# Kernel tuning notes

Hardware: AMD Instinct MI355X
Metric: run time of the kernel (lower is better)

## Reference

```python
import jax, jax.numpy as jnp
import numpy as np

BN_EPS = 1e-5

def setup_inputs() -> dict:
    key = jax.random.key(0)
    ks = jax.random.split(key, 12)
    B, C, H, W = 8, 512, 56, 56
    IC = 256  # inter_channels = in_channels // 2
    s_in = 1.0 / np.sqrt(C)
    s_ic = 1.0 / np.sqrt(IC)
    return {
        "x": jax.random.normal(ks[0], (B, C, H, W), dtype=jnp.float32),
        "theta_w": jax.random.normal(ks[1], (IC, C), dtype=jnp.float32) * s_in,
        "theta_b": jax.random.normal(ks[2], (IC,), dtype=jnp.float32) * s_in,
        "phi_w": jax.random.normal(ks[3], (IC, C), dtype=jnp.float32) * s_in,
        "phi_b": jax.random.normal(ks[4], (IC,), dtype=jnp.float32) * s_in,
        "g_w": jax.random.normal(ks[5], (IC, C), dtype=jnp.float32) * s_in,
        "g_b": jax.random.normal(ks[6], (IC,), dtype=jnp.float32) * s_in,
        "wz_w": jax.random.normal(ks[7], (C, IC), dtype=jnp.float32) * s_ic,
        "wz_b": jax.random.normal(ks[8], (C,), dtype=jnp.float32) * s_ic,
        "bn_w": jax.random.normal(ks[9], (C,), dtype=jnp.float32) * 0.1,
        "bn_b": jax.random.normal(ks[10], (C,), dtype=jnp.float32) * 0.1,
    }


def reference(x, theta_w, theta_b, phi_w, phi_b, g_w, g_b, wz_w, wz_b, bn_w, bn_b):
    B, C, H, W = x.shape
    N = H * W
    # [B, N, C] tokens
    xf = x.reshape(B, C, N).transpose(0, 2, 1)
    Q = jnp.einsum('bnc,ic->bni', xf, theta_w) + theta_b   # [B, N, IC]
    K = jnp.einsum('bnc,ic->bni', xf, phi_w) + phi_b       # [B, N, IC]
    V = jnp.einsum('bnc,ic->bni', xf, g_w) + g_b           # [B, N, IC]
    attn = jax.nn.softmax(jnp.einsum('bqi,bki->bqk', Q, K), axis=-1)  # [B, N, N]
    y = jnp.einsum('bqk,bki->bqi', attn, V)                # [B, N, IC]
    y = jnp.einsum('bqi,ci->bqc', y, wz_w) + wz_b          # [B, N, C]
    y = y.transpose(0, 2, 1).reshape(B, C, H, W)
    # BatchNorm2d, training-mode batch stats (biased variance)
    mean = jnp.mean(y, axis=(0, 2, 3))
    var = jnp.var(y, axis=(0, 2, 3))
    yn = (y - mean[None, :, None, None]) * jax.lax.rsqrt(var + BN_EPS)[None, :, None, None]
    y = yn * bn_w[None, :, None, None] + bn_b[None, :, None, None]
    return y + x
```

## Files before the change

kernel.cpp:

```cpp
#include <hip/hip_runtime.h>
#include <math.h>

#define B_  8
#define C_  512
#define N_  3136
#define IC_ 256
#define NPART 784

typedef __attribute__((ext_vector_type(8))) short bf16x8;
typedef __attribute__((ext_vector_type(4))) float f32x4;
typedef __attribute__((ext_vector_type(16))) float f32x16;

static __device__ __forceinline__ unsigned short f2bf(float f) {
    unsigned int u = __builtin_bit_cast(unsigned int, f);
    u = (u + 0x7fffu + ((u >> 16) & 1u)) >> 16;
    return (unsigned short)u;
}
static __device__ __forceinline__ float bf2f(unsigned short u) {
    return __builtin_bit_cast(float, (unsigned int)u << 16);
}
static __device__ __forceinline__ unsigned int pk2(float a, float b) {
    return (unsigned int)f2bf(a) | ((unsigned int)f2bf(b) << 16);
}

static __device__ __forceinline__ void gll16(const unsigned short* g, unsigned short* l) {
    __builtin_amdgcn_global_load_lds(
        (const __attribute__((address_space(1))) unsigned int*)g,
        (__attribute__((address_space(3))) unsigned int*)l, 16, 0, 0);
}

__global__ __launch_bounds__(256) void xpose_kernel(
    const float* __restrict__ x, unsigned short* __restrict__ xb)
{
    const int n0 = blockIdx.x * 64;
    const int c0 = blockIdx.y * 64;
    const int b  = blockIdx.z;
    __shared__ unsigned short T[64][72];
    const int tid = threadIdx.x;
#pragma unroll
    for (int e = 0; e < 4; ++e) {
        const int idx = tid + e * 256;
        const int row = idx >> 4;
        const int c4  = idx & 15;
        const float4 v = *(const float4*)&x[((size_t)b * C_ + c0 + row) * N_ + n0 + c4 * 4];
        T[c4 * 4 + 0][row] = f2bf(v.x);
        T[c4 * 4 + 1][row] = f2bf(v.y);
        T[c4 * 4 + 2][row] = f2bf(v.z);
        T[c4 * 4 + 3][row] = f2bf(v.w);
    }
    __syncthreads();
#pragma unroll
    for (int e = 0; e < 2; ++e) {
        const int s  = tid + e * 256;
        const int nr = s >> 3;
        const int sl = s & 7;
        *(bf16x8*)&xb[((size_t)b * N_ + n0 + nr) * C_ + c0 + sl * 8] =
            *(const bf16x8*)&T[nr][sl * 8];
    }
}

__global__ __launch_bounds__(256) void wconv_kernel(
    const float* __restrict__ tw, const float* __restrict__ pw,
    const float* __restrict__ gw, const float* __restrict__ wzw,
    unsigned short* __restrict__ Wcat, unsigned short* __restrict__ wzwb)
{
    const int gid = blockIdx.x * 256 + threadIdx.x;
    if (gid < 98304) {
        const int i  = gid >> 7;
        const int c4 = gid & 127;
        const float* src = (i < 256) ? &tw[(size_t)i * 512]
                         : (i < 512) ? &pw[(size_t)(i - 256) * 512]
                                     : &gw[(size_t)(i - 512) * 512];
        const float4 v = *(const float4*)&src[c4 * 4];
        ushort4 o; o.x = f2bf(v.x); o.y = f2bf(v.y); o.z = f2bf(v.z); o.w = f2bf(v.w);
        *(ushort4*)&Wcat[(size_t)i * 512 + c4 * 4] = o;
    } else {
        const int g2 = gid - 98304;
        const int r  = g2 >> 6;
        const int c4 = g2 & 63;
        const float4 v = *(const float4*)&wzw[(size_t)r * 256 + c4 * 4];
        ushort4 o; o.x = f2bf(v.x); o.y = f2bf(v.y); o.z = f2bf(v.z); o.w = f2bf(v.w);
        *(ushort4*)&wzwb[(size_t)r * 256 + c4 * 4] = o;
    }
}

__global__ __launch_bounds__(256, 2) void qkv_mfma_kernel(
    const unsigned short* __restrict__ xb, const unsigned short* __restrict__ Wcat,
    const float* __restrict__ tb, const float* __restrict__ pb,
    const float* __restrict__ gb,
    unsigned short* __restrict__ Q, unsigned short* __restrict__ K,
    unsigned short* __restrict__ Vt)
{
    const int n0 = blockIdx.x * 64;
    const int by = blockIdx.y;
    const int b  = blockIdx.z;
    const int i0 = by * 128;
    const int tid = threadIdx.x;
    const int wq = tid >> 6, lane = tid & 63;
    const int g = lane >> 4, c = lane & 15;
    const int wm = wq >> 1, wn = wq & 1;

    __shared__ unsigned short smem[12288];
    unsigned short* Asm = smem;
    unsigned short* Bsm = smem + 4096;

    const int srow = tid >> 3;
    const int ssl  = tid & 7;

    f32x4 acc[2][4];
#pragma unroll
    for (int mb = 0; mb < 2; ++mb)
#pragma unroll
        for (int nb = 0; nb < 4; ++nb) acc[mb][nb] = (f32x4){0.f, 0.f, 0.f, 0.f};

    bf16x8 ast[2], bst[4];
#pragma unroll
    for (int e = 0; e < 2; ++e) {
        const int row = srow + e * 32;
        ast[e] = *(const bf16x8*)&xb[((size_t)b * N_ + n0 + row) * C_ + ((ssl ^ (row & 7)) << 3)];
    }
#pragma unroll
    for (int e = 0; e < 4; ++e) {
        const int row = srow + e * 32;
        bst[e] = *(const bf16x8*)&Wcat[(size_t)(i0 + row) * C_ + ((ssl ^ (row & 7)) << 3)];
    }
#pragma unroll
    for (int e = 0; e < 2; ++e) *(bf16x8*)&Asm[(srow + e * 32) * 64 + ssl * 8] = ast[e];
#pragma unroll
    for (int e = 0; e < 4; ++e) *(bf16x8*)&Bsm[(srow + e * 32) * 64 + ssl * 8] = bst[e];
    __syncthreads();

    const int arow[2] = { wm * 32 + c, wm * 32 + 16 + c };
    const int brow[4] = { wn * 64 + c, wn * 64 + 16 + c, wn * 64 + 32 + c, wn * 64 + 48 + c };

    for (int s = 0; s < 8; ++s) {
        const int c0n = (s < 7) ? (s + 1) * 64 : s * 64;
#pragma unroll
        for (int e = 0; e < 2; ++e) {
            const int row = srow + e * 32;
            ast[e] = *(const bf16x8*)&xb[((size_t)b * N_ + n0 + row) * C_ + c0n + ((ssl ^ (row & 7)) << 3)];
        }
#pragma unroll
        for (int e = 0; e < 4; ++e) {
            const int row = srow + e * 32;
            bst[e] = *(const bf16x8*)&Wcat[(size_t)(i0 + row) * C_ + c0n + ((ssl ^ (row & 7)) << 3)];
        }
#pragma unroll
        for (int ks = 0; ks < 2; ++ks) {
            bf16x8 af[2], bfr[4];
            const int sl = ((ks << 2) | g);
#pragma unroll
            for (int mb = 0; mb < 2; ++mb)
                af[mb] = *(const bf16x8*)&Asm[arow[mb] * 64 + ((sl ^ (c & 7)) << 3)];
#pragma unroll
            for (int nb = 0; nb < 4; ++nb)
                bfr[nb] = *(const bf16x8*)&Bsm[brow[nb] * 64 + ((sl ^ (c & 7)) << 3)];
#pragma unroll
            for (int mb = 0; mb < 2; ++mb)
#pragma unroll
                for (int nb = 0; nb < 4; ++nb)
                    acc[mb][nb] = __builtin_amdgcn_mfma_f32_16x16x32_bf16(af[mb], bfr[nb], acc[mb][nb], 0, 0, 0);
        }
        __syncthreads();
#pragma unroll
        for (int e = 0; e < 2; ++e) *(bf16x8*)&Asm[(srow + e * 32) * 64 + ssl * 8] = ast[e];
#pragma unroll
        for (int e = 0; e < 4; ++e) *(bf16x8*)&Bsm[(srow + e * 32) * 64 + ssl * 8] = bst[e];
        __syncthreads();
    }

    const int proj = by >> 1;
    const float* bias = (proj == 0) ? tb : (proj == 1) ? pb : gb;
    const int icb = (by & 1) * 128;
    if (proj < 2) {
        unsigned short* out = (proj == 0) ? Q : K;
#pragma unroll
        for (int mb = 0; mb < 2; ++mb)
#pragma unroll
            for (int nb = 0; nb < 4; ++nb)
#pragma unroll
                for (int r = 0; r < 4; ++r) {
                    const int token = n0 + wm * 32 + mb * 16 + g * 4 + r;
                    const int ic = icb + wn * 64 + nb * 16 + c;
                    out[((size_t)b * N_ + token) * IC_ + ic] = f2bf(acc[mb][nb][r] + bias[ic]);
                }
    } else {
        unsigned short* T = smem;
#pragma unroll
        for (int mb = 0; mb < 2; ++mb)
#pragma unroll
            for (int nb = 0; nb < 4; ++nb)
#pragma unroll
                for (int r = 0; r < 4; ++r) {
                    const int il = wn * 64 + nb * 16 + c;
                    const int tl = wm * 32 + mb * 16 + g * 4 + r;
                    T[il * 72 + tl] = f2bf(acc[mb][nb][r] + bias[icb + il]);
                }
        __syncthreads();
#pragma unroll
        for (int e = 0; e < 4; ++e) {
            const int row = (tid >> 3) + e * 32;
            *(bf16x8*)&Vt[((size_t)b * IC_ + icb + row) * N_ + n0 + ((tid & 7) * 8)] =
                *(const bf16x8*)&T[row * 72 + (tid & 7) * 8];
        }
    }
}

__global__ __launch_bounds__(512, 2) void attn_kernel(
    const unsigned short* __restrict__ Q, const unsigned short* __restrict__ K,
    const unsigned short* __restrict__ Vt,
    unsigned short* __restrict__ part, float2* __restrict__ ml)
{
    const int b     = blockIdx.x;
    const int qb    = blockIdx.y;
    const int split = blockIdx.z;
    int q0 = qb * 256; if (q0 > N_ - 256) q0 = N_ - 256;
    const int t0 = split ? 25 : 0;
    const int t1 = split ? 49 : 25;

    const int tid  = threadIdx.x;
    const int wq   = tid >> 6;
    const int lane = tid & 63;
    const int ql   = lane & 31;
    const int h    = lane >> 5;
    const int swz0 = (ql & 7) ^ (ql >> 3);

    const unsigned short* Qb = Q  + (size_t)b * N_ * IC_;
    const unsigned short* Kb = K  + (size_t)b * N_ * IC_;
    const unsigned short* Vb = Vt + (size_t)b * IC_ * N_;

    __shared__ unsigned short Ks[2][64 * 256];
    __shared__ unsigned short Vs[2][256 * 64];

    const int krow = tid >> 5, ksl = tid & 31;
    const int vrow = tid >> 3, vsl = tid & 7;
    const unsigned short* vg =
        Vb + (size_t)vrow * N_ + ((vsl ^ ((vrow & 7) ^ ((vrow >> 3) & 7))) << 3);

#define STAGE(buf, t)                                                            \
    {                                                                            \
        _Pragma("unroll") for (int e = 0; e < 4; ++e) {                          \
            const int kr = krow + e * 16;                                        \
            gll16(Kb + ((size_t)(t) * 64 + kr) * IC_ +                           \
                      ((ksl ^ ((kr & 7) ^ ((kr >> 3) & 7))) << 3),               \
                  &Ks[buf][(tid + e * 512) * 8]);                                \
        }                                                                        \
        const unsigned short* vgp = vg + (size_t)(t) * 64;                       \
        _Pragma("unroll") for (int e = 0; e < 4; ++e)                            \
            gll16(vgp + (size_t)e * 64 * N_, &Vs[buf][(tid + e * 512) * 8]);     \
    }

    bf16x8 qf[16];
    {
        const unsigned short* qrow = &Qb[(size_t)(q0 + wq * 32 + ql) * IC_ + h * 8];
#pragma unroll
        for (int s = 0; s < 16; ++s) qf[s] = *(const bf16x8*)&qrow[s * 16];
    }

    f32x16 yacc[8];
#pragma unroll
    for (int db = 0; db < 8; ++db)
#pragma unroll
        for (int i = 0; i < 16; ++i) yacc[db][i] = 0.f;
    float m = -1e30f, lsum = 0.f;

    STAGE(0, t0);
    asm volatile("s_waitcnt vmcnt(0)" ::: "memory");
    __syncthreads();

    for (int t = t0; t < t1; ++t) {
        const int cur = (t - t0) & 1;
        if (t + 1 < t1) STAGE(cur ^ 1, t + 1);

        f32x16 s0, s1;
#pragma unroll
        for (int i = 0; i < 16; ++i) { s0[i] = 0.f; s1[i] = 0.f; }
        __builtin_amdgcn_s_setprio(1);
#pragma unroll
        for (int s = 0; s < 16; ++s) {
            const int sl = ((2 * s + h) ^ swz0) << 3;
            const bf16x8 kf0 = *(const bf16x8*)&Ks[cur][(size_t)ql * 256 + sl];
            s0 = __builtin_amdgcn_mfma_f32_32x32x16_bf16(kf0, qf[s], s0, 0, 0, 0);
            const bf16x8 kf1 = *(const bf16x8*)&Ks[cur][(size_t)(32 + ql) * 256 + (sl ^ 32)];
            s1 = __builtin_amdgcn_mfma_f32_32x32x16_bf16(kf1, qf[s], s1, 0, 0, 0);
        }
        __builtin_amdgcn_s_setprio(0);

        float mx[16];
#pragma unroll
        for (int i = 0; i < 16; ++i) mx[i] = fmaxf(s0[i], s1[i]);
#pragma unroll
        for (int off = 8; off > 0; off >>= 1)
#pragma unroll
            for (int i = 0; i < 8; ++i)
                if (i < off) mx[i] = fmaxf(mx[i], mx[i + off]);
        float rm = fmaxf(mx[0], __shfl_xor(mx[0], 32));

        if (__any(rm > m + 8.f)) {
            const float mnew  = fmaxf(m, rm);
            const float scale = __expf(m - mnew);
            m = mnew;
            lsum *= scale;
#pragma unroll
            for (int db = 0; db < 8; ++db)
#pragma unroll
                for (int i = 0; i < 16; ++i) yacc[db][i] *= scale;
        }

#pragma unroll
        for (int i = 0; i < 16; ++i) s0[i] = __expf(s0[i] - m);
#pragma unroll
        for (int i = 0; i < 16; ++i) s1[i] = __expf(s1[i] - m);
        float sm[16];
#pragma unroll
        for (int i = 0; i < 16; ++i) sm[i] = s0[i] + s1[i];
#pragma unroll
        for (int off = 8; off > 0; off >>= 1)
#pragma unroll
            for (int i = 0; i < 8; ++i)
                if (i < off) sm[i] += sm[i + off];
        lsum += sm[0] + __shfl_xor(sm[0], 32);

        unsigned int pk0[8], pk1[8];
#pragma unroll
        for (int w = 0; w < 8; ++w) {
            pk0[w] = pk2(s0[2 * w], s0[2 * w + 1]);
            pk1[w] = pk2(s1[2 * w], s1[2 * w + 1]);
        }

#pragma unroll
        for (int s = 0; s < 4; ++s) {
            const unsigned int* u4 = (s >> 1) ? &pk1[4 * (s & 1)] : &pk0[4 * (s & 1)];
            const unsigned int send0 = h ? u4[0] : u4[2];
            const unsigned int send1 = h ? u4[1] : u4[3];
            const unsigned int r0 = (unsigned int)__shfl_xor((int)send0, 32);
            const unsigned int r1 = (unsigned int)__shfl_xor((int)send1, 32);
            uint4 fw;
            fw.x = h ? r0 : u4[0];
            fw.y = h ? r1 : u4[1];
            fw.z = h ? u4[2] : r0;
            fw.w = h ? u4[3] : r1;
            const bf16x8 pf = __builtin_bit_cast(bf16x8, fw);
            const int vsl_r = ((2 * s + h) ^ swz0) << 3;
            __builtin_amdgcn_s_setprio(1);
#pragma unroll
            for (int db = 0; db < 8; ++db) {
                const bf16x8 vf = *(const bf16x8*)
                    &Vs[cur][(size_t)(db * 32 + ql) * 64 + (vsl_r ^ (((db & 1) << 2) << 3))];
                yacc[db] = __builtin_amdgcn_mfma_f32_32x32x16_bf16(vf, pf, yacc[db], 0, 0, 0);
            }
            __builtin_amdgcn_s_setprio(0);
        }

        asm volatile("s_waitcnt vmcnt(0)" ::: "memory");
        __syncthreads();
    }

    const size_t pbase = (size_t)(b * 2 + split) * N_;
    const int q = q0 + wq * 32 + ql;
    if (h == 0) ml[pbase + q] = make_float2(m, lsum);
#pragma unroll
    for (int db = 0; db < 8; ++db)
#pragma unroll
        for (int rq = 0; rq < 4; ++rq) {
            ushort4 o;
            o.x = f2bf(yacc[db][4 * rq + 0]);
            o.y = f2bf(yacc[db][4 * rq + 1]);
            o.z = f2bf(yacc[db][4 * rq + 2]);
            o.w = f2bf(yacc[db][4 * rq + 3]);
            *(ushort4*)&part[(pbase + q) * IC_ + 32 * db + 8 * rq + 4 * h] = o;
        }
#undef STAGE
}

__global__ __launch_bounds__(256) void attn_merge_kernel(
    const unsigned short* __restrict__ part, const float2* __restrict__ ml,
    unsigned short* __restrict__ Y)
{
    const int b  = blockIdx.y;
    const int q  = blockIdx.x * 64 + (threadIdx.x >> 2);
    const int d0 = (threadIdx.x & 3) * 64;
    const float2 A  = ml[(size_t)(b * 2 + 0) * N_ + q];
    const float2 Bv = ml[(size_t)(b * 2 + 1) * N_ + q];
    const float mm = fmaxf(A.x, Bv.x);
    const float wA = __expf(A.x - mm), wB = __expf(Bv.x - mm);
    const float inv = 1.f / (A.y * wA + Bv.y * wB);
    const unsigned short* pA = &part[((size_t)(b * 2 + 0) * N_ + q) * IC_ + d0];
    const unsigned short* pB = &part[((size_t)(b * 2 + 1) * N_ + q) * IC_ + d0];
    unsigned short* y = &Y[((size_t)b * N_ + q) * IC_ + d0];
#pragma unroll
    for (int j = 0; j < 8; ++j) {
        const bf16x8 va = *(const bf16x8*)&pA[j * 8];
        const bf16x8 vb = *(const bf16x8*)&pB[j * 8];
        unsigned short o[8];
#pragma unroll
        for (int k = 0; k < 8; ++k)
            o[k] = f2bf((bf2f((unsigned short)va[k]) * wA +
                         bf2f((unsigned short)vb[k]) * wB) * inv);
        *(bf16x8*)&y[j * 8] = *(const bf16x8*)o;
    }
}

__global__ __launch_bounds__(256, 2) void wz_mfma_kernel(
    const unsigned short* __restrict__ Yb, const unsigned short* __restrict__ wzwb,
    const float* __restrict__ wzb, float* __restrict__ Z,
    float2* __restrict__ partial)
{
    const int n0 = blockIdx.x * 64;
    const int c0 = blockIdx.y * 128;
    const int b  = blockIdx.z;
    const int tid = threadIdx.x;
    const int wq = tid >> 6, lane = tid & 63;
    const int g = lane >> 4, c = lane & 15;
    const int wm = wq >> 1, wn = wq & 1;

    __shared__ unsigned short smem[12288];
    unsigned short* Asm = smem;
    unsigned short* Bsm = smem + 8192;

    const int srow = tid >> 3;
    const int ssl  = tid & 7;

    f32x4 acc[4][2];
#pragma unroll
    for (int mb = 0; mb < 4; ++mb)
#pragma unroll
        for (int nb = 0; nb < 2; ++nb) acc[mb][nb] = (f32x4){0.f, 0.f, 0.f, 0.f};

    bf16x8 ast[4], bst[2];
#pragma unroll
    for (int e = 0; e < 4; ++e) {
        const int row = srow + e * 32;
        ast[e] = *(const bf16x8*)&wzwb[(size_t)(c0 + row) * IC_ + ((ssl ^ (row & 7)) << 3)];
    }
#pragma unroll
    for (int e = 0; e < 2; ++e) {
        const int row = srow + e * 32;
        bst[e] = *(const bf16x8*)&Yb[((size_t)b * N_ + n0 + row) * IC_ + ((ssl ^ (row & 7)) << 3)];
    }
#pragma unroll
    for (int e = 0; e < 4; ++e) *(bf16x8*)&Asm[(srow + e * 32) * 64 + ssl * 8] = ast[e];
#pragma unroll
    for (int e = 0; e < 2; ++e) *(bf16x8*)&Bsm[(srow + e * 32) * 64 + ssl * 8] = bst[e];
    __syncthreads();

    const int arow[4] = { wm * 64 + c, wm * 64 + 16 + c, wm * 64 + 32 + c, wm * 64 + 48 + c };
    const int brow[2] = { wn * 32 + c, wn * 32 + 16 + c };

    for (int s = 0; s < 4; ++s) {
        const int k0n = (s < 3) ? (s + 1) * 64 : s * 64;
#pragma unroll
        for (int e = 0; e < 4; ++e) {
            const int row = srow + e * 32;
            ast[e] = *(const bf16x8*)&wzwb[(size_t)(c0 + row) * IC_ + k0n + ((ssl ^ (row & 7)) << 3)];
        }
#pragma unroll
        for (int e = 0; e < 2; ++e) {
            const int row = srow + e * 32;
            bst[e] = *(const bf16x8*)&Yb[((size_t)b * N_ + n0 + row) * IC_ + k0n + ((ssl ^ (row & 7)) << 3)];
        }
#pragma unroll
        for (int ks = 0; ks < 2; ++ks) {
            bf16x8 af[4], bfr[2];
            const int sl = ((ks << 2) | g);
#pragma unroll
            for (int mb = 0; mb < 4; ++mb)
                af[mb] = *(const bf16x8*)&Asm[arow[mb] * 64 + ((sl ^ (c & 7)) << 3)];
#pragma unroll
            for (int nb = 0; nb < 2; ++nb)
                bfr[nb] = *(const bf16x8*)&Bsm[brow[nb] * 64 + ((sl ^ (c & 7)) << 3)];
#pragma unroll
            for (int mb = 0; mb < 4; ++mb)
#pragma unroll
                for (int nb = 0; nb < 2; ++nb)
                    acc[mb][nb] = __builtin_amdgcn_mfma_f32_16x16x32_bf16(af[mb], bfr[nb], acc[mb][nb], 0, 0, 0);
        }
        __syncthreads();
#pragma unroll
        for (int e = 0; e < 4; ++e) *(bf16x8*)&Asm[(srow + e * 32) * 64 + ssl * 8] = ast[e];
#pragma unroll
        for (int e = 0; e < 2; ++e) *(bf16x8*)&Bsm[(srow + e * 32) * 64 + ssl * 8] = bst[e];
        __syncthreads();
    }

    const int slot = (b * 49 + blockIdx.x) * 2 + wn;
#pragma unroll
    for (int mb = 0; mb < 4; ++mb) {
#pragma unroll
        for (int r = 0; r < 4; ++r) {
            const int cg = c0 + wm * 64 + mb * 16 + g * 4 + r;
            const float bw = wzb[cg];
            const float z0 = acc[mb][0][r] + bw;
            const float z1 = acc[mb][1][r] + bw;
            Z[((size_t)b * C_ + cg) * N_ + n0 + wn * 32 + c]      = z0;
            Z[((size_t)b * C_ + cg) * N_ + n0 + wn * 32 + 16 + c] = z1;
            float ps = z0 + z1;
            float pq = z0 * z0 + z1 * z1;
#pragma unroll
            for (int off = 1; off <= 8; off <<= 1) {
                ps += __shfl_xor(ps, off);
                pq += __shfl_xor(pq, off);
            }
            if (c == 0) partial[(size_t)cg * NPART + slot] = make_float2(ps, pq);
        }
    }
}

__global__ __launch_bounds__(256) void bn_finalize_kernel(
    const float2* __restrict__ partial, float* __restrict__ stats)
{
    const int c   = blockIdx.x;
    const int tid = threadIdx.x;
    double s = 0.0, q = 0.0;
    for (int i = tid; i < NPART; i += 256) {
        const float2 p = partial[(size_t)c * NPART + i];
        s += p.x; q += p.y;
    }
    __shared__ double ls[256], lq[256];
    ls[tid] = s; lq[tid] = q;
    __syncthreads();
    for (int off = 128; off > 0; off >>= 1) {
        if (tid < off) { ls[tid] += ls[tid + off]; lq[tid] += lq[tid + off]; }
        __syncthreads();
    }
    if (tid == 0) {
        const double M    = (double)B_ * (double)N_;
        const double mean = ls[0] / M;
        const double var  = lq[0] / M - mean * mean;
        stats[c]      = (float)mean;
        stats[C_ + c] = (float)var;
    }
}

__global__ __launch_bounds__(256) void bn_apply_kernel(
    const float* __restrict__ Z, const float* __restrict__ x,
    const float* __restrict__ stats,
    const float* __restrict__ bnw, const float* __restrict__ bnb,
    float* __restrict__ out)
{
    const size_t total4 = (size_t)B_ * C_ * N_ / 4;
    const size_t i4 = (size_t)blockIdx.x * blockDim.x + threadIdx.x;
    if (i4 >= total4) return;
    const size_t i = i4 * 4;
    const int c = (int)((i / N_) % C_);
    const float mean = stats[c];
    const float var  = stats[C_ + c];
    const float sc = rsqrtf(var + 1e-5f) * bnw[c];
    const float sh = bnb[c] - mean * sc;
    const float4 z  = ((const float4*)Z)[i4];
    const float4 xv = ((const float4*)x)[i4];
    float4 o;
    o.x = z.x * sc + sh + xv.x;
    o.y = z.y * sc + sh + xv.y;
    o.z = z.z * sc + sh + xv.z;
    o.w = z.w * sc + sh + xv.w;
    ((float4*)out)[i4] = o;
}

extern "C" void kernel_launch(void* const* d_in, const int* in_sizes, int n_in,
                              void* d_out, int out_size, void* d_ws, size_t ws_size,
                              hipStream_t stream)
{
    const float* x   = (const float*)d_in[0];
    const float* tw  = (const float*)d_in[1];
    const float* tb  = (const float*)d_in[2];
    const float* pw  = (const float*)d_in[3];
    const float* pb  = (const float*)d_in[4];
    const float* gw  = (const float*)d_in[5];
    const float* gb  = (const float*)d_in[6];
    const float* wzw = (const float*)d_in[7];
    const float* wzb = (const float*)d_in[8];
    const float* bnw = (const float*)d_in[9];
    const float* bnb = (const float*)d_in[10];
    float* out = (float*)d_out;

    const size_t NIC = (size_t)B_ * N_ * IC_;
    const size_t BNC = (size_t)B_ * N_ * C_;
    unsigned short* Qw   = (unsigned short*)d_ws;
    unsigned short* Kw   = Qw + NIC;
    unsigned short* Vtw  = Kw + NIC;
    unsigned short* Ybw  = Vtw + NIC;
    unsigned short* xbw  = Ybw + NIC;
    unsigned short* partw = xbw;
    unsigned short* Wcat = xbw + BNC;
    unsigned short* wzwb = Wcat + 768 * 512;
    float* stats = (float*)(wzwb + 512 * 256);
    float2* mlw  = (float2*)(stats + 2 * C_);
    float2* bnpart = mlw + (size_t)B_ * 2 * N_;
    float* Zb    = out;

    wconv_kernel<<<512, 256, 0, stream>>>(tw, pw, gw, wzw, Wcat, wzwb);
    xpose_kernel<<<dim3(N_ / 64, C_ / 64, B_), 256, 0, stream>>>(x, xbw);
    qkv_mfma_kernel<<<dim3(N_ / 64, 6, B_), 256, 0, stream>>>(
        xbw, Wcat, tb, pb, gb, Qw, Kw, Vtw);
    attn_kernel<<<dim3(B_, 13, 2), 512, 0, stream>>>(Qw, Kw, Vtw, partw, mlw);
    attn_merge_kernel<<<dim3(N_ / 64, B_), 256, 0, stream>>>(partw, mlw, Ybw);
    wz_mfma_kernel<<<dim3(N_ / 64, C_ / 128, B_), 256, 0, stream>>>(Ybw, wzwb, wzb, Zb, bnpart);
    bn_finalize_kernel<<<C_, 256, 0, stream>>>(bnpart, stats);
    const int total4 = B_ * C_ * N_ / 4;
    bn_apply_kernel<<<(total4 + 255) / 256, 256, 0, stream>>>(Zb, x, stats, bnw, bnb, out);
}
```

Before: 273.2 us.

## Split attention into four KV splits with smaller query blocks, single-buffered LDS

The attention kernel moves from 512-thread blocks over 256 queries with a 2-way KV split to 256-thread blocks over 128 queries with a 4-way KV split (13/12/12/12 tiles). The grid grows from 208 to 800 blocks, which fills more CUs. Shared memory drops from double-buffered to a single buffer, so each tile's load is no longer overlapped with compute and the loop now syncs twice per tile. The merge kernel combines four partials, one of them written in place into the output buffer, which adds extra partial-buffer traffic and workspace.

After: 438.2 us. 60.4% more time.

```diff
diff --git a/kernel.cpp b/kernel.cpp
--- a/kernel.cpp
+++ b/kernel.cpp
@@ -206,17 +206,19 @@
     }
 }
 
-__global__ __launch_bounds__(512, 2) void attn_kernel(
+__global__ __launch_bounds__(256, 2) void attn_kernel(
     const unsigned short* __restrict__ Q, const unsigned short* __restrict__ K,
     const unsigned short* __restrict__ Vt,
-    unsigned short* __restrict__ part, float2* __restrict__ ml)
+    unsigned short* __restrict__ p0, unsigned short* __restrict__ p1,
+    unsigned short* __restrict__ p2, unsigned short* __restrict__ p3,
+    float2* __restrict__ ml)
 {
     const int b     = blockIdx.x;
     const int qb    = blockIdx.y;
     const int split = blockIdx.z;
-    int q0 = qb * 256; if (q0 > N_ - 256) q0 = N_ - 256;
-    const int t0 = split ? 25 : 0;
-    const int t1 = split ? 49 : 25;
+    int q0 = qb * 128; if (q0 > N_ - 128) q0 = N_ - 128;
+    const int t0 = split * 12 + (split ? 1 : 0);
+    const int t1 = t0 + (split ? 12 : 13);
 
     const int tid  = threadIdx.x;
     const int wq   = tid >> 6;
@@ -229,25 +231,26 @@
     const unsigned short* Kb = K  + (size_t)b * N_ * IC_;
     const unsigned short* Vb = Vt + (size_t)b * IC_ * N_;
 
-    __shared__ unsigned short Ks[2][64 * 256];
-    __shared__ unsigned short Vs[2][256 * 64];
-
-    const int krow = tid >> 5, ksl = tid & 31;
-    const int vrow = tid >> 3, vsl = tid & 7;
-    const unsigned short* vg =
-        Vb + (size_t)vrow * N_ + ((vsl ^ ((vrow & 7) ^ ((vrow >> 3) & 7))) << 3);
-
-#define STAGE(buf, t)                                                            \
-    {                                                                            \
-        _Pragma("unroll") for (int e = 0; e < 4; ++e) {                          \
-            const int kr = krow + e * 16;                                        \
-            gll16(Kb + ((size_t)(t) * 64 + kr) * IC_ +                           \
-                      ((ksl ^ ((kr & 7) ^ ((kr >> 3) & 7))) << 3),               \
-                  &Ks[buf][(tid + e * 512) * 8]);                                \
-        }                                                                        \
-        const unsigned short* vgp = vg + (size_t)(t) * 64;                       \
-        _Pragma("unroll") for (int e = 0; e < 4; ++e)                            \
-            gll16(vgp + (size_t)e * 64 * N_, &Vs[buf][(tid + e * 512) * 8]);     \
+    __shared__ unsigned short Ks[64 * 256];
+    __shared__ unsigned short Vs[256 * 64];
+
+    const int ksl = tid & 31;
+    const int vsl = tid & 7;
+
+#define STAGE(t)                                                               \
+    {                                                                          \
+        _Pragma("unroll") for (int e = 0; e < 8; ++e) {                        \
+            const int kr = (tid >> 5) + e * 8;                                 \
+            gll16(Kb + ((size_t)(t) * 64 + kr) * IC_ +                         \
+                      ((ksl ^ ((kr & 7) ^ ((kr >> 3) & 7))) << 3),             \
+                  &Ks[(tid + e * 256) * 8]);                                   \
+        }                                                                      \
+        _Pragma("unroll") for (int e = 0; e < 8; ++e) {                        \
+            const int vr = (tid >> 3) + e * 32;                                \
+            gll16(Vb + (size_t)vr * N_ + (size_t)(t) * 64 +                    \
+                      ((vsl ^ ((vr & 7) ^ ((vr >> 3) & 7))) << 3),             \
+                  &Vs[(tid + e * 256) * 8]);                                   \
+        }                                                                      \
     }
 
     bf16x8 qf[16];
@@ -264,13 +267,11 @@
         for (int i = 0; i < 16; ++i) yacc[db][i] = 0.f;
     float m = -1e30f, lsum = 0.f;
 
-    STAGE(0, t0);
-    asm volatile("s_waitcnt vmcnt(0)" ::: "memory");
-    __syncthreads();
-
     for (int t = t0; t < t1; ++t) {
-        const int cur = (t - t0) & 1;
-        if (t + 1 < t1) STAGE(cur ^ 1, t + 1);
+        __syncthreads();
+        STAGE(t);
+        asm volatile("s_waitcnt vmcnt(0)" ::: "memory");
+        __syncthreads();
 
         f32x16 s0, s1;
 #pragma unroll
@@ -279,9 +280,9 @@
 #pragma unroll
         for (int s = 0; s < 16; ++s) {
             const int sl = ((2 * s + h) ^ swz0) << 3;
-            const bf16x8 kf0 = *(const bf16x8*)&Ks[cur][(size_t)ql * 256 + sl];
+            const bf16x8 kf0 = *(const bf16x8*)&Ks[(size_t)ql * 256 + sl];
             s0 = __builtin_amdgcn_mfma_f32_32x32x16_bf16(kf0, qf[s], s0, 0, 0, 0);
-            const bf16x8 kf1 = *(const bf16x8*)&Ks[cur][(size_t)(32 + ql) * 256 + (sl ^ 32)];
+            const bf16x8 kf1 = *(const bf16x8*)&Ks[(size_t)(32 + ql) * 256 + (sl ^ 32)];
             s1 = __builtin_amdgcn_mfma_f32_32x32x16_bf16(kf1, qf[s], s1, 0, 0, 0);
         }
         __builtin_amdgcn_s_setprio(0);
@@ -346,19 +347,16 @@
 #pragma unroll
             for (int db = 0; db < 8; ++db) {
                 const bf16x8 vf = *(const bf16x8*)
-                    &Vs[cur][(size_t)(db * 32 + ql) * 64 + (vsl_r ^ (((db & 1) << 2) << 3))];
+                    &Vs[(size_t)(db * 32 + ql) * 64 + (vsl_r ^ (((db & 1) << 2) << 3))];
                 yacc[db] = __builtin_amdgcn_mfma_f32_32x32x16_bf16(vf, pf, yacc[db], 0, 0, 0);
             }
             __builtin_amdgcn_s_setprio(0);
         }
-
-        asm volatile("s_waitcnt vmcnt(0)" ::: "memory");
-        __syncthreads();
-    }
-
-    const size_t pbase = (size_t)(b * 2 + split) * N_;
+    }
+
+    unsigned short* part = (split == 0) ? p0 : (split == 1) ? p1 : (split == 2) ? p2 : p3;
     const int q = q0 + wq * 32 + ql;
-    if (h == 0) ml[pbase + q] = make_float2(m, lsum);
+    if (h == 0) ml[(size_t)(split * B_ + b) * N_ + q] = make_float2(m, lsum);
 #pragma unroll
     for (int db = 0; db < 8; ++db)
 #pragma unroll
@@ -368,35 +366,46 @@
             o.y = f2bf(yacc[db][4 * rq + 1]);
             o.z = f2bf(yacc[db][4 * rq + 2]);
             o.w = f2bf(yacc[db][4 * rq + 3]);
-            *(ushort4*)&part[(pbase + q) * IC_ + 32 * db + 8 * rq + 4 * h] = o;
+            *(ushort4*)&part[((size_t)b * N_ + q) * IC_ + 32 * db + 8 * rq + 4 * h] = o;
         }
 #undef STAGE
 }
 
 __global__ __launch_bounds__(256) void attn_merge_kernel(
-    const unsigned short* __restrict__ part, const float2* __restrict__ ml,
-    unsigned short* __restrict__ Y)
+    const unsigned short* p0, const unsigned short* p1,
+    const unsigned short* p2, const unsigned short* p3,
+    const float2* __restrict__ ml, unsigned short* Y)
 {
     const int b  = blockIdx.y;
     const int q  = blockIdx.x * 64 + (threadIdx.x >> 2);
     const int d0 = (threadIdx.x & 3) * 64;
-    const float2 A  = ml[(size_t)(b * 2 + 0) * N_ + q];
-    const float2 Bv = ml[(size_t)(b * 2 + 1) * N_ + q];
-    const float mm = fmaxf(A.x, Bv.x);
-    const float wA = __expf(A.x - mm), wB = __expf(Bv.x - mm);
-    const float inv = 1.f / (A.y * wA + Bv.y * wB);
-    const unsigned short* pA = &part[((size_t)(b * 2 + 0) * N_ + q) * IC_ + d0];
-    const unsigned short* pB = &part[((size_t)(b * 2 + 1) * N_ + q) * IC_ + d0];
-    unsigned short* y = &Y[((size_t)b * N_ + q) * IC_ + d0];
+    float2 s0 = ml[(size_t)(0 * B_ + b) * N_ + q];
+    float2 s1 = ml[(size_t)(1 * B_ + b) * N_ + q];
+    float2 s2 = ml[(size_t)(2 * B_ + b) * N_ + q];
+    float2 s3 = ml[(size_t)(3 * B_ + b) * N_ + q];
+    const float mm = fmaxf(fmaxf(s0.x, s1.x), fmaxf(s2.x, s3.x));
+    const float w0 = __expf(s0.x - mm), w1 = __expf(s1.x - mm);
+    const float w2 = __expf(s2.x - mm), w3 = __expf(s3.x - mm);
+    const float inv = 1.f / (s0.y * w0 + s1.y * w1 + s2.y * w2 + s3.y * w3);
+    const size_t base = ((size_t)b * N_ + q) * IC_ + d0;
+    const unsigned short* pa = p0 + base;
+    const unsigned short* pb = p1 + base;
+    const unsigned short* pc = p2 + base;
+    const unsigned short* pd = p3 + base;
+    unsigned short* y = Y + base;
 #pragma unroll
     for (int j = 0; j < 8; ++j) {
-        const bf16x8 va = *(const bf16x8*)&pA[j * 8];
-        const bf16x8 vb = *(const bf16x8*)&pB[j * 8];
+        const bf16x8 va = *(const bf16x8*)&pa[j * 8];
+        const bf16x8 vb = *(const bf16x8*)&pb[j * 8];
+        const bf16x8 vc = *(const bf16x8*)&pc[j * 8];
+        const bf16x8 vd = *(const bf16x8*)&pd[j * 8];
         unsigned short o[8];
 #pragma unroll
         for (int k = 0; k < 8; ++k)
-            o[k] = f2bf((bf2f((unsigned short)va[k]) * wA +
-                         bf2f((unsigned short)vb[k]) * wB) * inv);
+            o[k] = f2bf((bf2f((unsigned short)va[k]) * w0 +
+                         bf2f((unsigned short)vb[k]) * w1 +
+                         bf2f((unsigned short)vc[k]) * w2 +
+                         bf2f((unsigned short)vd[k]) * w3) * inv);
         *(bf16x8*)&y[j * 8] = *(const bf16x8*)o;
     }
 }
@@ -581,20 +590,24 @@
     unsigned short* Vtw  = Kw + NIC;
     unsigned short* Ybw  = Vtw + NIC;
     unsigned short* xbw  = Ybw + NIC;
-    unsigned short* partw = xbw;
+    unsigned short* p1w  = xbw;
+    unsigned short* p2w  = xbw + NIC;
     unsigned short* Wcat = xbw + BNC;
     unsigned short* wzwb = Wcat + 768 * 512;
     float* stats = (float*)(wzwb + 512 * 256);
     float2* mlw  = (float2*)(stats + 2 * C_);
-    float2* bnpart = mlw + (size_t)B_ * 2 * N_;
+    float2* bnpart = mlw + (size_t)4 * B_ * N_;
+    unsigned short* p3w = (unsigned short*)(bnpart + (size_t)C_ * NPART);
     float* Zb    = out;
 
     wconv_kernel<<<512, 256, 0, stream>>>(tw, pw, gw, wzw, Wcat, wzwb);
     xpose_kernel<<<dim3(N_ / 64, C_ / 64, B_), 256, 0, stream>>>(x, xbw);
     qkv_mfma_kernel<<<dim3(N_ / 64, 6, B_), 256, 0, stream>>>(
         xbw, Wcat, tb, pb, gb, Qw, Kw, Vtw);
-    attn_kernel<<<dim3(B_, 13, 2), 512, 0, stream>>>(Qw, Kw, Vtw, partw, mlw);
-    attn_merge_kernel<<<dim3(N_ / 64, B_), 256, 0, stream>>>(partw, mlw, Ybw);
+    attn_kernel<<<dim3(B_, 25, 4), 256, 0, stream>>>(
+        Qw, Kw, Vtw, Ybw, p1w, p2w, p3w, mlw);
+    attn_merge_kernel<<<dim3(N_ / 64, B_), 256, 0, stream>>>(
+        Ybw, p1w, p2w, p3w, mlw, Ybw);
     wz_mfma_kernel<<<dim3(N_ / 64, C_ / 128, B_), 256, 0, stream>>>(Ybw, wzwb, wzb, Zb, bnpart);
     bn_finalize_kernel<<<C_, 256, 0, stream>>>(bnpart, stats);
     const int total4 = B_ * C_ * N_ / 4;
```

## Software-pipeline attention loop: overlap PV of previous tile with QK and softmax of current

Applied to the files above, without the earlier changes.

Restructures the flash-attention inner loop so the P·V MFMAs for tile t-1 are issued after the QK and exp of tile t, giving the exp/reduction work independent MFMA work to overlap with. K becomes single-buffered while V uses a triple buffer so the previous tile's V stays resident. The online-softmax rescale is applied after the deferred PV, and also to the current exp values, so accumulation stays consistent. This adds a prologue and epilogue, an extra barrier per iteration and more live registers (packed P values), which may reduce occupancy or cause spills.

New measurement: 388.4 us. 1.42x slower.

```diff
diff --git a/kernel.cpp b/kernel.cpp
--- a/kernel.cpp
+++ b/kernel.cpp
@@ -229,25 +229,67 @@
     const unsigned short* Kb = K  + (size_t)b * N_ * IC_;
     const unsigned short* Vb = Vt + (size_t)b * IC_ * N_;
 
-    __shared__ unsigned short Ks[2][64 * 256];
-    __shared__ unsigned short Vs[2][256 * 64];
+    __shared__ unsigned short Ks[64 * 256];
+    __shared__ unsigned short Vs[3][256 * 64];
 
     const int krow = tid >> 5, ksl = tid & 31;
     const int vrow = tid >> 3, vsl = tid & 7;
     const unsigned short* vg =
         Vb + (size_t)vrow * N_ + ((vsl ^ ((vrow & 7) ^ ((vrow >> 3) & 7))) << 3);
 
-#define STAGE(buf, t)                                                            \
+#define STAGE_K(t)                                                               \
     {                                                                            \
         _Pragma("unroll") for (int e = 0; e < 4; ++e) {                          \
             const int kr = krow + e * 16;                                        \
             gll16(Kb + ((size_t)(t) * 64 + kr) * IC_ +                           \
                       ((ksl ^ ((kr & 7) ^ ((kr >> 3) & 7))) << 3),               \
-                  &Ks[buf][(tid + e * 512) * 8]);                                \
+                  &Ks[(tid + e * 512) * 8]);                                     \
         }                                                                        \
+    }
+#define STAGE_V(slot, t)                                                         \
+    {                                                                            \
         const unsigned short* vgp = vg + (size_t)(t) * 64;                       \
+        unsigned short* vdst = &Vs[slot][0];                                     \
         _Pragma("unroll") for (int e = 0; e < 4; ++e)                            \
-            gll16(vgp + (size_t)e * 64 * N_, &Vs[buf][(tid + e * 512) * 8]);     \
+            gll16(vgp + (size_t)e * 64 * N_, &vdst[(tid + e * 512) * 8]);        \
+    }
+
+#define QK_BLOCK()                                                               \
+    {                                                                            \
+        __builtin_amdgcn_s_setprio(1);                                           \
+        _Pragma("unroll") for (int s = 0; s < 16; ++s) {                         \
+            const int sl = ((2 * s + h) ^ swz0) << 3;                            \
+            const bf16x8 kf0 = *(const bf16x8*)&Ks[(size_t)ql * 256 + sl];       \
+            s0 = __builtin_amdgcn_mfma_f32_32x32x16_bf16(kf0, qf[s], s0, 0, 0, 0); \
+            const bf16x8 kf1 = *(const bf16x8*)&Ks[(size_t)(32 + ql) * 256 + (sl ^ 32)]; \
+            s1 = __builtin_amdgcn_mfma_f32_32x32x16_bf16(kf1, qf[s], s1, 0, 0, 0); \
+        }                                                                        \
+        __builtin_amdgcn_s_setprio(0);                                           \
+    }
+
+#define PV_BLOCK(vslot)                                                          \
+    {                                                                            \
+        _Pragma("unroll") for (int s = 0; s < 4; ++s) {                          \
+            const unsigned int* u4 = (s >> 1) ? &pk1[4 * (s & 1)] : &pk0[4 * (s & 1)]; \
+            const unsigned int send0 = h ? u4[0] : u4[2];                        \
+            const unsigned int send1 = h ? u4[1] : u4[3];                        \
+            const unsigned int r0 = (unsigned int)__shfl_xor((int)send0, 32);    \
+            const unsigned int r1 = (unsigned int)__shfl_xor((int)send1, 32);    \
+            uint4 fw;                                                            \
+            fw.x = h ? r0 : u4[0];                                               \
+            fw.y = h ? r1 : u4[1];                                               \
+            fw.z = h ? u4[2] : r0;                                               \
+            fw.w = h ? u4[3] : r1;                                               \
+            const bf16x8 pf = __builtin_bit_cast(bf16x8, fw);                    \
+            const int vsl_r = ((2 * s + h) ^ swz0) << 3;                         \
+            __builtin_amdgcn_s_setprio(1);                                       \
+            _Pragma("unroll") for (int db = 0; db < 8; ++db) {                   \
+                const bf16x8 vf = *(const bf16x8*)                               \
+                    &Vs[vslot][(size_t)(db * 32 + ql) * 64 + (vsl_r ^ (((db & 1) << 2) << 3))]; \
+                yacc[db] = __builtin_amdgcn_mfma_f32_32x32x16_bf16(vf, pf, yacc[db], 0, 0, 0); \
+            }                                                                    \
+            __builtin_amdgcn_s_setprio(0);                                       \
+        }                                                                        \
     }
 
     bf16x8 qf[16];
@@ -262,29 +304,22 @@
     for (int db = 0; db < 8; ++db)
 #pragma unroll
         for (int i = 0; i < 16; ++i) yacc[db][i] = 0.f;
-    float m = -1e30f, lsum = 0.f;
-
-    STAGE(0, t0);
+    float m, lsum;
+    unsigned int pk0[8], pk1[8];
+
+    STAGE_K(t0);
+    STAGE_V(0, t0);
     asm volatile("s_waitcnt vmcnt(0)" ::: "memory");
     __syncthreads();
 
-    for (int t = t0; t < t1; ++t) {
-        const int cur = (t - t0) & 1;
-        if (t + 1 < t1) STAGE(cur ^ 1, t + 1);
-
+    {
         f32x16 s0, s1;
 #pragma unroll
         for (int i = 0; i < 16; ++i) { s0[i] = 0.f; s1[i] = 0.f; }
-        __builtin_amdgcn_s_setprio(1);
-#pragma unroll
-        for (int s = 0; s < 16; ++s) {
-            const int sl = ((2 * s + h) ^ swz0) << 3;
-            const bf16x8 kf0 = *(const bf16x8*)&Ks[cur][(size_t)ql * 256 + sl];
-            s0 = __builtin_amdgcn_mfma_f32_32x32x16_bf16(kf0, qf[s], s0, 0, 0, 0);
-            const bf16x8 kf1 = *(const bf16x8*)&Ks[cur][(size_t)(32 + ql) * 256 + (sl ^ 32)];
-            s1 = __builtin_amdgcn_mfma_f32_32x32x16_bf16(kf1, qf[s], s1, 0, 0, 0);
-        }
-        __builtin_amdgcn_s_setprio(0);
+        QK_BLOCK();
+        __syncthreads();
+        STAGE_K(t0 + 1);
+        STAGE_V(1, t0 + 1);
 
         float mx[16];
 #pragma unroll
@@ -294,66 +329,98 @@
 #pragma unroll
             for (int i = 0; i < 8; ++i)
                 if (i < off) mx[i] = fmaxf(mx[i], mx[i + off]);
-        float rm = fmaxf(mx[0], __shfl_xor(mx[0], 32));
-
+        m = fmaxf(mx[0], __shfl_xor(mx[0], 32));
+
+#pragma unroll
+        for (int i = 0; i < 16; ++i) s0[i] = __expf(s0[i] - m);
+#pragma unroll
+        for (int i = 0; i < 16; ++i) s1[i] = __expf(s1[i] - m);
+        float sm[16];
+#pragma unroll
+        for (int i = 0; i < 16; ++i) sm[i] = s0[i] + s1[i];
+#pragma unroll
+        for (int off = 8; off > 0; off >>= 1)
+#pragma unroll
+            for (int i = 0; i < 8; ++i)
+                if (i < off) sm[i] += sm[i + off];
+        lsum = sm[0] + __shfl_xor(sm[0], 32);
+
+#pragma unroll
+        for (int w = 0; w < 8; ++w) {
+            pk0[w] = pk2(s0[2 * w], s0[2 * w + 1]);
+            pk1[w] = pk2(s1[2 * w], s1[2 * w + 1]);
+        }
+        asm volatile("s_waitcnt vmcnt(0)" ::: "memory");
+        __syncthreads();
+    }
+
+    int vcur = 1;
+    for (int t = t0 + 1; t < t1; ++t) {
+        const int vprev = (vcur == 0) ? 2 : vcur - 1;
+        const int vnext = (vcur == 2) ? 0 : vcur + 1;
+
+        f32x16 s0, s1;
+#pragma unroll
+        for (int i = 0; i < 16; ++i) { s0[i] = 0.f; s1[i] = 0.f; }
+        QK_BLOCK();
+        __syncthreads();
+        if (t + 1 < t1) { STAGE_K(t + 1); STAGE_V(vnext, t + 1); }
+
+        float mx[16];
+#pragma unroll
+        for (int i = 0; i < 16; ++i) mx[i] = fmaxf(s0[i], s1[i]);
+#pragma unroll
+        for (int off = 8; off > 0; off >>= 1)
+#pragma unroll
+            for (int i = 0; i < 8; ++i)
+                if (i < off) mx[i] = fmaxf(mx[i], mx[i + off]);
+
+#pragma unroll
+        for (int i = 0; i < 16; ++i) s0[i] = __expf(s0[i] - m);
+#pragma unroll
+        for (int i = 0; i < 16; ++i) s1[i] = __expf(s1[i] - m);
+        float sm[16];
+#pragma unroll
+        for (int i = 0; i < 16; ++i) sm[i] = s0[i] + s1[i];
+#pragma unroll
+        for (int off = 8; off > 0; off >>= 1)
+#pragma unroll
+            for (int i = 0; i < 8; ++i)
+                if (i < off) sm[i] += sm[i + off];
+
+        PV_BLOCK(vprev);
+
+        const float rm  = fmaxf(mx[0], __shfl_xor(mx[0], 32));
+        const float prt = sm[0] + __shfl_xor(sm[0], 32);
         if (__any(rm > m + 8.f)) {
             const float mnew  = fmaxf(m, rm);
             const float scale = __expf(m - mnew);
             m = mnew;
-            lsum *= scale;
+            lsum = (lsum + prt) * scale;
+#pragma unroll
+            for (int i = 0; i < 16; ++i) { s0[i] *= scale; s1[i] *= scale; }
 #pragma unroll
             for (int db = 0; db < 8; ++db)
 #pragma unroll
                 for (int i = 0; i < 16; ++i) yacc[db][i] *= scale;
-        }
-
-#pragma unroll
-        for (int i = 0; i < 16; ++i) s0[i] = __expf(s0[i] - m);
-#pragma unroll
-        for (int i = 0; i < 16; ++i) s1[i] = __expf(s1[i] - m);
-        float sm[16];
-#pragma unroll
-        for (int i = 0; i < 16; ++i) sm[i] = s0[i] + s1[i];
-#pragma unroll
-        for (int off = 8; off > 0; off >>= 1)
-#pragma unroll
-            for (int i = 0; i < 8; ++i)
-                if (i < off) sm[i] += sm[i + off];
-        lsum += sm[0] + __shfl_xor(sm[0], 32);
-
-        unsigned int pk0[8], pk1[8];
+        } else {
+            lsum += prt;
+        }
+
 #pragma unroll
         for (int w = 0; w < 8; ++w) {
             pk0[w] = pk2(s0[2 * w], s0[2 * w + 1]);
             pk1[w] = pk2(s1[2 * w], s1[2 * w + 1]);
         }
 
-#pragma unroll
-        for (int s = 0; s < 4; ++s) {
-            const unsigned int* u4 = (s >> 1) ? &pk1[4 * (s & 1)] : &pk0[4 * (s & 1)];
-            const unsigned int send0 = h ? u4[0] : u4[2];
-            const unsigned int send1 = h ? u4[1] : u4[3];
-            const unsigned int r0 = (unsigned int)__shfl_xor((int)send0, 32);
-            const unsigned int r1 = (unsigned int)__shfl_xor((int)send1, 32);
-            uint4 fw;
-            fw.x = h ? r0 : u4[0];
-            fw.y = h ? r1 : u4[1];
-            fw.z = h ? u4[2] : r0;
-            fw.w = h ? u4[3] : r1;
-            const bf16x8 pf = __builtin_bit_cast(bf16x8, fw);
-            const int vsl_r = ((2 * s + h) ^ swz0) << 3;
-            __builtin_amdgcn_s_setprio(1);
-#pragma unroll
-            for (int db = 0; db < 8; ++db) {
-                const bf16x8 vf = *(const bf16x8*)
-                    &Vs[cur][(size_t)(db * 32 + ql) * 64 + (vsl_r ^ (((db & 1) << 2) << 3))];
-                yacc[db] = __builtin_amdgcn_mfma_f32_32x32x16_bf16(vf, pf, yacc[db], 0, 0, 0);
-            }
-            __builtin_amdgcn_s_setprio(0);
-        }
-
         asm volatile("s_waitcnt vmcnt(0)" ::: "memory");
         __syncthreads();
+        vcur = vnext;
+    }
+
+    {
+        const int vlast = (vcur == 0) ? 2 : vcur - 1;
+        PV_BLOCK(vlast);
     }
 
     const size_t pbase = (size_t)(b * 2 + split) * N_;
@@ -370,7 +437,10 @@
             o.w = f2bf(yacc[db][4 * rq + 3]);
             *(ushort4*)&part[(pbase + q) * IC_ + 32 * db + 8 * rq + 4 * h] = o;
         }
-#undef STAGE
+#undef STAGE_K
+#undef STAGE_V
+#undef QK_BLOCK
+#undef PV_BLOCK
 }
 
 __global__ __launch_bounds__(256) void attn_merge_kernel(
```
